# Performance work log

Hardware: AMD Instinct MI355X
Metric: run time of the kernel (lower is better)

Reference implementation:

```python
import jax, jax.numpy as jnp
import numpy as np

N = 50000        # num nodes
E = 800000       # num edges (avg degree 16)
NFEAT = 128
NHID = 128
NCLASS = 64


def setup_inputs() -> dict:
    key = jax.random.key(0)
    k0, k1, k2, k3 = jax.random.split(key, 4)
    x = jax.random.normal(k0, (N, NFEAT), dtype=jnp.float32)
    edge_index = jax.random.randint(k1, (2, E), 0, N)
    edge_weight = jnp.ones((E,), dtype=jnp.float32)
    # GCNConv linear weights (glorot-ish uniform), biases zero
    s1 = 1.0 / np.sqrt(NFEAT)
    W1 = jax.random.uniform(k2, (NFEAT, NHID), jnp.float32, -s1, s1)
    b1 = jnp.zeros((NHID,), jnp.float32)
    s2 = 1.0 / np.sqrt(NHID)
    W2 = jax.random.uniform(k3, (NHID, NCLASS), jnp.float32, -s2, s2)
    b2 = jnp.zeros((NCLASS,), jnp.float32)
    return {"x": x, "edge_index": edge_index, "edge_weight": edge_weight,
            "W1": W1, "b1": b1, "W2": W2, "b2": b2}


def reference(x, edge_index, edge_weight, W1, b1, W2, b2):
    n = x.shape[0]
    # add self loops (fill_value = 1.0), as GCNConv(add_self_loops=True)
    loops = jnp.arange(n)
    ei = jnp.concatenate([edge_index, jnp.stack([loops, loops])], axis=1)
    ew = jnp.concatenate([edge_weight, jnp.ones((n,), x.dtype)])
    row, col = ei[0], ei[1]
    # symmetric gcn normalization: D^-1/2 A D^-1/2
    deg = jax.ops.segment_sum(ew, col, num_segments=n)
    dinv = jnp.where(deg > 0, jax.lax.rsqrt(deg), 0.0)
    norm = dinv[row] * ew * dinv[col]        # [E+N]

    def conv(h, W, b):
        h = h @ W                                   # [N, F_out]
        msg = norm[:, None] * h[row]                # gather + scale, [E+N, F_out]
        return jax.ops.segment_sum(msg, col, num_segments=n) + b

    h = jax.nn.relu(conv(x, W1, b1))  # dropout p=0.0 -> identity
    out = conv(h, W2, b2)
    # F.normalize(p=2, dim=-1)
    nrm = jnp.linalg.norm(out, axis=-1, keepdims=True)
    return out / jnp.maximum(nrm, 1e-12)
```

## Files before the change

### kernel.cpp

```cpp
#include <hip/hip_runtime.h>

#define NF 128
#define NC 64
#define SLICES 64

__device__ __forceinline__ unsigned f2bf(float f) {
    unsigned u = __float_as_uint(f);
    return (u + 0x7FFFu + ((u >> 16) & 1u)) >> 16;
}
__device__ __forceinline__ float bf2f(unsigned h) { return __uint_as_float(h << 16); }

__global__ __launch_bounds__(256) void count_rank_kernel(const int* __restrict__ col,
                                                         unsigned short* __restrict__ eoff16,
                                                         unsigned short* __restrict__ C16,
                                                         int N, int E, int SL, int nh) {
    __shared__ unsigned hist[12544];
    const int j = blockIdx.x >> 1;
    const int h = blockIdx.x & 1;
    const int nlo = h * nh;
    const int nhi = min(N, nlo + nh);
    const int words = (nhi - nlo + 1) >> 1;
    for (int i = threadIdx.x; i < words; i += 256) hist[i] = 0;
    __syncthreads();
    const int e0 = j * SL, e1 = min(E, e0 + SL);
    for (int e = e0 + threadIdx.x; e < e1; e += 256) {
        int c = col[e];
        if (c >= nlo && c < nhi) {
            int cl = c - nlo;
            unsigned sh = (cl & 1) * 16;
            unsigned old = atomicAdd(&hist[cl >> 1], 1u << sh);
            eoff16[e] = (unsigned short)((old >> sh) & 0xffffu);
        }
    }
    __syncthreads();
    unsigned* Cw = (unsigned*)(C16 + (size_t)j * N + nlo);
    for (int i = threadIdx.x; i < words; i += 256) Cw[i] = hist[i];
}

__global__ __launch_bounds__(256) void scanC_kernel(unsigned short* __restrict__ C16,
                                                    int* __restrict__ tot, int N) {
    int n = blockIdx.x * 256 + threadIdx.x;
    if (n >= N) return;
    int t = 0;
#pragma unroll 4
    for (int j = 0; j < SLICES; ++j) {
        size_t idx = (size_t)j * N + n;
        int v = C16[idx];
        C16[idx] = (unsigned short)t;
        t += v;
    }
    tot[n] = t;
}

__global__ __launch_bounds__(256) void scan_blocks(const int* __restrict__ cnt,
                                                   int* __restrict__ excl,
                                                   int* __restrict__ bsum, int N) {
    __shared__ int sh[256];
    int t = threadIdx.x;
    int base = blockIdx.x * 1024 + t * 4;
    int v0 = base + 0 < N ? cnt[base + 0] : 0;
    int v1 = base + 1 < N ? cnt[base + 1] : 0;
    int v2 = base + 2 < N ? cnt[base + 2] : 0;
    int v3 = base + 3 < N ? cnt[base + 3] : 0;
    int s = v0 + v1 + v2 + v3;
    sh[t] = s;
    __syncthreads();
    for (int off = 1; off < 256; off <<= 1) {
        int x = (t >= off) ? sh[t - off] : 0;
        __syncthreads();
        sh[t] += x;
        __syncthreads();
    }
    int incl = sh[t];
    int exclT = incl - s;
    if (t == 255) bsum[blockIdx.x] = incl;
    if (base + 0 < N) excl[base + 0] = exclT;
    if (base + 1 < N) excl[base + 1] = exclT + v0;
    if (base + 2 < N) excl[base + 2] = exclT + v0 + v1;
    if (base + 3 < N) excl[base + 3] = exclT + v0 + v1 + v2;
}

__global__ void scan_sums(int* __restrict__ bsum, int nb) {
    int run = 0;
    for (int i = 0; i < nb; ++i) { int v = bsum[i]; bsum[i] = run; run += v; }
    bsum[nb] = run;
}

__global__ __launch_bounds__(256) void scan_add(int* __restrict__ excl,
                                                const int* __restrict__ bsum,
                                                int N, int nb) {
    int i = blockIdx.x * 256 + threadIdx.x;
    if (i < N) excl[i] += bsum[i >> 10];
    if (i == 0) excl[N] = bsum[nb];
}

__global__ __launch_bounds__(256) void scatter_gemm1_fused(const int* __restrict__ row,
                                                           const int* __restrict__ col,
                                                           const float* __restrict__ ew,
                                                           const int* __restrict__ rowPtr,
                                                           const unsigned short* __restrict__ Coff16,
                                                           const unsigned short* __restrict__ eoff16,
                                                           int2* __restrict__ csr,
                                                           const float* __restrict__ X,
                                                           const float* __restrict__ W,
                                                           unsigned short* __restrict__ H,
                                                           int N, int E, int SL, int SB) {
    __shared__ float Xs[32][64];
    __shared__ float Wsh[32][128];
    if ((int)blockIdx.x < SB) {
        int stride = SB * 256;
        for (int e = blockIdx.x * 256 + threadIdx.x; e < E; e += stride) {
            int c = col[e];
            int j = e / SL;
            int idx = rowPtr[c] + (int)Coff16[(size_t)j * N + c] + (int)eoff16[e];
            csr[idx] = make_int2(row[e], __float_as_int(ew[e]));
        }
        return;
    }
    const int bm0 = (blockIdx.x - SB) * 64;
    const int tid = threadIdx.x;
    const int tx = tid & 15, ty = tid >> 4;
    float acc[4][8] = {};
    for (int kc = 0; kc < 4; ++kc) {
        {
            int r = tid >> 2, q = tid & 3;
            int node = min(bm0 + r, N - 1);
            const float4* src = (const float4*)(X + (size_t)node * 128 + kc * 32);
#pragma unroll
            for (int qq = 0; qq < 2; ++qq) {
                float4 v = src[q + qq * 4];
                int k = (q + qq * 4) * 4;
                Xs[k + 0][r] = v.x;
                Xs[k + 1][r] = v.y;
                Xs[k + 2][r] = v.z;
                Xs[k + 3][r] = v.w;
            }
        }
        {
            const float4* src = (const float4*)(W + (size_t)kc * 32 * 128);
            float4* dst = (float4*)&Wsh[0][0];
#pragma unroll
            for (int i = tid; i < 1024; i += 256) dst[i] = src[i];
        }
        __syncthreads();
#pragma unroll 4
        for (int k = 0; k < 32; ++k) {
            float4 xa = *(const float4*)&Xs[k][tx * 4];
            float4 wA = *(const float4*)&Wsh[k][ty * 8];
            float4 wB = *(const float4*)&Wsh[k][ty * 8 + 4];
            float xv[4] = {xa.x, xa.y, xa.z, xa.w};
            float wv[8] = {wA.x, wA.y, wA.z, wA.w, wB.x, wB.y, wB.z, wB.w};
#pragma unroll
            for (int i = 0; i < 4; ++i)
#pragma unroll
                for (int j = 0; j < 8; ++j)
                    acc[i][j] = fmaf(xv[i], wv[j], acc[i][j]);
        }
        __syncthreads();
    }
#pragma unroll
    for (int i = 0; i < 4; ++i) {
        int n = bm0 + tx * 4 + i;
        if (n < N) {
            ushort4 oA, oB;
            oA.x = (unsigned short)f2bf(acc[i][0]); oA.y = (unsigned short)f2bf(acc[i][1]);
            oA.z = (unsigned short)f2bf(acc[i][2]); oA.w = (unsigned short)f2bf(acc[i][3]);
            oB.x = (unsigned short)f2bf(acc[i][4]); oB.y = (unsigned short)f2bf(acc[i][5]);
            oB.z = (unsigned short)f2bf(acc[i][6]); oB.w = (unsigned short)f2bf(acc[i][7]);
            *(ushort4*)&H[(size_t)n * 128 + ty * 8] = oA;
            *(ushort4*)&H[(size_t)n * 128 + ty * 8 + 4] = oB;
        }
    }
}

__global__ __launch_bounds__(256) void deg_dinv_kernel(const int* __restrict__ rowPtr,
                                                       const int2* __restrict__ csr,
                                                       float* __restrict__ dinv, int N) {
    int idx = blockIdx.x * 256 + threadIdx.x;
    int n = idx >> 4, l = idx & 15;
    if (n >= N) return;
    int beg = rowPtr[n], end = rowPtr[n + 1];
    float s = 0.f;
    for (int i = beg + l; i < end; i += 16) s += __int_as_float(csr[i].y);
#pragma unroll
    for (int off = 8; off; off >>= 1) s += __shfl_xor(s, off, 16);
    if (l == 0) dinv[n] = rsqrtf(s + 1.0f);
}

__global__ __launch_bounds__(256) void norm_csr_kernel(int2* __restrict__ csr,
                                                       const float* __restrict__ dinv, int E) {
    int i = blockIdx.x * 256 + threadIdx.x;
    if (i >= E) return;
    int2 p = csr[i];
    ((int*)csr)[2 * i + 1] = __float_as_int(__int_as_float(p.y) * dinv[p.x]);
}

__global__ __launch_bounds__(256) void agg_gather1(const int* __restrict__ rowPtr,
                                                   const int2* __restrict__ csr,
                                                   const unsigned* __restrict__ H1u,
                                                   const float* __restrict__ dinv,
                                                   const float2* __restrict__ b2,
                                                   float2* __restrict__ out2, int N) {
    int n = (blockIdx.x * 256 + threadIdx.x) >> 6;
    int lane = threadIdx.x & 63;
    if (n >= N) return;
    float dn = dinv[n];
    float accx = 0.f, accy = 0.f;
    int beg = rowPtr[n], end = rowPtr[n + 1];
    int j = beg;
    for (; j + 4 <= end; j += 4) {
        int2 p0 = csr[j + 0], p1 = csr[j + 1], p2 = csr[j + 2], p3 = csr[j + 3];
        unsigned v0 = H1u[(size_t)p0.x * 64 + lane];
        unsigned v1 = H1u[(size_t)p1.x * 64 + lane];
        unsigned v2 = H1u[(size_t)p2.x * 64 + lane];
        unsigned v3 = H1u[(size_t)p3.x * 64 + lane];
        float w0 = __int_as_float(p0.y), w1 = __int_as_float(p1.y);
        float w2 = __int_as_float(p2.y), w3 = __int_as_float(p3.y);
        accx += w0 * bf2f(v0 & 0xffffu); accy += w0 * bf2f(v0 >> 16);
        accx += w1 * bf2f(v1 & 0xffffu); accy += w1 * bf2f(v1 >> 16);
        accx += w2 * bf2f(v2 & 0xffffu); accy += w2 * bf2f(v2 >> 16);
        accx += w3 * bf2f(v3 & 0xffffu); accy += w3 * bf2f(v3 >> 16);
    }
    for (; j < end; ++j) {
        int2 p = csr[j];
        unsigned v = H1u[(size_t)p.x * 64 + lane];
        float w = __int_as_float(p.y);
        accx += w * bf2f(v & 0xffffu); accy += w * bf2f(v >> 16);
    }
    unsigned hv = H1u[(size_t)n * 64 + lane];
    float2 bb = b2[lane];
    float s = dn * dn;
    float2 o;
    o.x = fmaxf(fmaf(dn, accx, s * bf2f(hv & 0xffffu)) + bb.x, 0.f);
    o.y = fmaxf(fmaf(dn, accy, s * bf2f(hv >> 16)) + bb.y, 0.f);
    out2[(size_t)n * 64 + lane] = o;
}

__global__ __launch_bounds__(256) void gemm_tile64(const float* __restrict__ X,
                                                   const float* __restrict__ W,
                                                   unsigned short* __restrict__ H, int N) {
    __shared__ float Xs[32][64];
    __shared__ float Wsh[32][64];
    const int bm0 = blockIdx.x * 64;
    const int tid = threadIdx.x;
    const int tx = tid & 15, ty = tid >> 4;
    float acc[4][4] = {};
    for (int kc = 0; kc < 4; ++kc) {
        {
            int r = tid >> 2, q = tid & 3;
            int node = min(bm0 + r, N - 1);
            const float4* src = (const float4*)(X + (size_t)node * 128 + kc * 32);
#pragma unroll
            for (int qq = 0; qq < 2; ++qq) {
                float4 v = src[q + qq * 4];
                int k = (q + qq * 4) * 4;
                Xs[k + 0][r] = v.x;
                Xs[k + 1][r] = v.y;
                Xs[k + 2][r] = v.z;
                Xs[k + 3][r] = v.w;
            }
        }
        {
            const float4* src = (const float4*)(W + (size_t)kc * 32 * 64);
            float4* dst = (float4*)&Wsh[0][0];
#pragma unroll
            for (int i = tid; i < 512; i += 256) dst[i] = src[i];
        }
        __syncthreads();
#pragma unroll 4
        for (int k = 0; k < 32; ++k) {
            float4 xa = *(const float4*)&Xs[k][tx * 4];
            float4 w4 = *(const float4*)&Wsh[k][ty * 4];
            float xv[4] = {xa.x, xa.y, xa.z, xa.w};
            float wv[4] = {w4.x, w4.y, w4.z, w4.w};
#pragma unroll
            for (int i = 0; i < 4; ++i)
#pragma unroll
                for (int j = 0; j < 4; ++j)
                    acc[i][j] = fmaf(xv[i], wv[j], acc[i][j]);
        }
        __syncthreads();
    }
#pragma unroll
    for (int i = 0; i < 4; ++i) {
        int n = bm0 + tx * 4 + i;
        if (n < N) {
            ushort4 o;
            o.x = (unsigned short)f2bf(acc[i][0]);
            o.y = (unsigned short)f2bf(acc[i][1]);
            o.z = (unsigned short)f2bf(acc[i][2]);
            o.w = (unsigned short)f2bf(acc[i][3]);
            *(ushort4*)&H[(size_t)n * 64 + ty * 4] = o;
        }
    }
}

__global__ __launch_bounds__(256) void agg_gather2(const int* __restrict__ rowPtr,
                                                   const int2* __restrict__ csr,
                                                   const unsigned* __restrict__ H3u,
                                                   const float* __restrict__ dinv,
                                                   const float2* __restrict__ b2,
                                                   float2* __restrict__ out2, int N) {
    int n = (blockIdx.x * 256 + threadIdx.x) >> 5;
    int l = threadIdx.x & 31;
    if (n >= N) return;
    float dn = dinv[n];
    float accx = 0.f, accy = 0.f;
    int beg = rowPtr[n], end = rowPtr[n + 1];
    int j = beg;
    for (; j + 4 <= end; j += 4) {
        int2 p0 = csr[j + 0], p1 = csr[j + 1], p2 = csr[j + 2], p3 = csr[j + 3];
        unsigned v0 = H3u[(size_t)p0.x * 32 + l];
        unsigned v1 = H3u[(size_t)p1.x * 32 + l];
        unsigned v2 = H3u[(size_t)p2.x * 32 + l];
        unsigned v3 = H3u[(size_t)p3.x * 32 + l];
        float w0 = __int_as_float(p0.y), w1 = __int_as_float(p1.y);
        float w2 = __int_as_float(p2.y), w3 = __int_as_float(p3.y);
        accx += w0 * bf2f(v0 & 0xffffu); accy += w0 * bf2f(v0 >> 16);
        accx += w1 * bf2f(v1 & 0xffffu); accy += w1 * bf2f(v1 >> 16);
        accx += w2 * bf2f(v2 & 0xffffu); accy += w2 * bf2f(v2 >> 16);
        accx += w3 * bf2f(v3 & 0xffffu); accy += w3 * bf2f(v3 >> 16);
    }
    for (; j < end; ++j) {
        int2 p = csr[j];
        unsigned v = H3u[(size_t)p.x * 32 + l];
        float w = __int_as_float(p.y);
        accx += w * bf2f(v & 0xffffu); accy += w * bf2f(v >> 16);
    }
    unsigned hv = H3u[(size_t)n * 32 + l];
    float2 bb = b2[l];
    float s = dn * dn;
    float vx = fmaf(dn, accx, s * bf2f(hv & 0xffffu)) + bb.x;
    float vy = fmaf(dn, accy, s * bf2f(hv >> 16)) + bb.y;
    float ss = vx * vx + vy * vy;
#pragma unroll
    for (int off = 16; off; off >>= 1) ss += __shfl_xor(ss, off, 64);
    float scale = 1.0f / fmaxf(sqrtf(ss), 1e-12f);
    out2[(size_t)n * 32 + l] = make_float2(vx * scale, vy * scale);
}

extern "C" void kernel_launch(void* const* d_in, const int* in_sizes, int n_in,
                              void* d_out, int out_size, void* d_ws, size_t ws_size,
                              hipStream_t stream) {
    const float* x  = (const float*)d_in[0];
    const int*   ei = (const int*)d_in[1];
    const float* ew = (const float*)d_in[2];
    const float* W1 = (const float*)d_in[3];
    const float* b1 = (const float*)d_in[4];
    const float* W2 = (const float*)d_in[5];
    const float* b2 = (const float*)d_in[6];
    float* out = (float*)d_out;
    const int N = in_sizes[0] / NF;
    const int E = in_sizes[2];
    const int* row = ei;
    const int* col = ei + E;
    const int NB = (N + 1023) / 1024;
    const int SL = (E + SLICES - 1) / SLICES;
    const int nh = (N + 1) / 2;

    char* ws = (char*)d_ws;
    size_t off = 0;
    auto take = [&](size_t bytes) {
        char* p = ws + off;
        off = (off + bytes + 255) & ~(size_t)255;
        return p;
    };
    float* dinv   = (float*)take((size_t)N * 4);
    int*   tot    = (int*)  take((size_t)N * 4);
    int*   rowPtr = (int*)  take((size_t)(N + 1) * 4);
    unsigned short* eoff16 = (unsigned short*)take((size_t)E * 2);
    int*   bsum   = (int*)  take((size_t)(NB + 1) * 4);
    unsigned short* C16    = (unsigned short*)take((size_t)SLICES * N * 2);
    int2*  csr    = (int2*) take((size_t)E * 8);
    unsigned short* H1 = (unsigned short*)take((size_t)N * NF * 2);
    float* buf2   = (float*)take((size_t)N * NF * 4);
    unsigned short* H3 = H1;

    count_rank_kernel<<<2 * SLICES, 256, 0, stream>>>(col, eoff16, C16, N, E, SL, nh);
    scanC_kernel<<<(N + 255) / 256, 256, 0, stream>>>(C16, tot, N);
    scan_blocks<<<NB, 256, 0, stream>>>(tot, rowPtr, bsum, N);
    scan_sums<<<1, 1, 0, stream>>>(bsum, NB);
    scan_add<<<(N + 255) / 256, 256, 0, stream>>>(rowPtr, bsum, N, NB);

    const int SB = 128;
    const int GB = (N + 63) / 64;
    scatter_gemm1_fused<<<SB + GB, 256, 0, stream>>>(row, col, ew, rowPtr, C16, eoff16,
                                                     csr, x, W1, H1, N, E, SL, SB);

    deg_dinv_kernel<<<(N * 16 + 255) / 256, 256, 0, stream>>>(rowPtr, csr, dinv, N);
    norm_csr_kernel<<<(E + 255) / 256, 256, 0, stream>>>(csr, dinv, E);

    agg_gather1<<<(N * 64 + 255) / 256, 256, 0, stream>>>(rowPtr, csr, (const unsigned*)H1,
                                                          dinv, (const float2*)b1,
                                                          (float2*)buf2, N);

    gemm_tile64<<<(N + 63) / 64, 256, 0, stream>>>(buf2, W2, H3, N);
    agg_gather2<<<(N * 32 + 255) / 256, 256, 0, stream>>>(rowPtr, csr, (const unsigned*)H3,
                                                          dinv, (const float2*)b2,
                                                          (float2*)out, N);
}
```

Baseline: 174.4 us.

## Use bf16 MFMA for both GEMMs, fold normalization into gathers, partition scatter

Both dense GEMMs move from scalar FP32 FMA tiles to bf16 MFMA 16x16x32 tiles. The inputs are converted to bf16 into swizzled LDS, and the weights are pre-transposed to bf16 by a new prep kernel. The separate norm_csr pass is removed, so each gather multiplies by dinv[src] on the fly. The layer-1 ReLU output is stored as bf16 instead of fp32, halving the GEMM2 input traffic. The CSR scatter blocks are split into four node-range quarters to improve write locality, at the cost of each block rereading all of col. Lower input precision and the extra dinv gathers are the tradeoffs.

```diff
diff --git a/kernel.cpp b/kernel.cpp
--- a/kernel.cpp
+++ b/kernel.cpp
@@ -4,11 +4,31 @@
 #define NC 64
 #define SLICES 64
 
+typedef short bf16x8 __attribute__((ext_vector_type(8)));
+typedef float f32x4 __attribute__((ext_vector_type(4)));
+
 __device__ __forceinline__ unsigned f2bf(float f) {
     unsigned u = __float_as_uint(f);
     return (u + 0x7FFFu + ((u >> 16) & 1u)) >> 16;
 }
 __device__ __forceinline__ float bf2f(unsigned h) { return __uint_as_float(h << 16); }
+
+__global__ __launch_bounds__(256) void wt_prep(const float* __restrict__ W1,
+                                               const float* __restrict__ W2,
+                                               unsigned short* __restrict__ Wt1,
+                                               unsigned short* __restrict__ Wt2) {
+    int i = blockIdx.x * 256 + threadIdx.x;
+    if (i < 128 * 128) {
+        int k = i >> 7, n = i & 127;
+        Wt1[n * 128 + k] = (unsigned short)f2bf(W1[i]);
+    } else {
+        int j = i - 128 * 128;
+        if (j < 128 * 64) {
+            int k = j >> 6, n = j & 63;
+            Wt2[n * 128 + k] = (unsigned short)f2bf(W2[j]);
+        }
+    }
+}
 
 __global__ __launch_bounds__(256) void count_rank_kernel(const int* __restrict__ col,
                                                          unsigned short* __restrict__ eoff16,
@@ -102,75 +122,141 @@
                                                            const unsigned short* __restrict__ eoff16,
                                                            int2* __restrict__ csr,
                                                            const float* __restrict__ X,
-                                                           const float* __restrict__ W,
+                                                           const unsigned short* __restrict__ Wt1,
                                                            unsigned short* __restrict__ H,
-                                                           int N, int E, int SL, int SB) {
-    __shared__ float Xs[32][64];
-    __shared__ float Wsh[32][128];
+                                                           int N, int E, int SL, int SB, int nq) {
+    __shared__ char XsB[32768];
+    __shared__ char WsB[32768];
     if ((int)blockIdx.x < SB) {
-        int stride = SB * 256;
-        for (int e = blockIdx.x * 256 + threadIdx.x; e < E; e += stride) {
+        int q = blockIdx.x & 3;
+        int qlo = q * nq, qhi = min(N, qlo + nq);
+        int stride = (SB >> 2) * 256;
+        for (int e = (blockIdx.x >> 2) * 256 + threadIdx.x; e < E; e += stride) {
             int c = col[e];
+            if (c < qlo || c >= qhi) continue;
             int j = e / SL;
             int idx = rowPtr[c] + (int)Coff16[(size_t)j * N + c] + (int)eoff16[e];
             csr[idx] = make_int2(row[e], __float_as_int(ew[e]));
         }
         return;
     }
-    const int bm0 = (blockIdx.x - SB) * 64;
     const int tid = threadIdx.x;
-    const int tx = tid & 15, ty = tid >> 4;
-    float acc[4][8] = {};
-    for (int kc = 0; kc < 4; ++kc) {
-        {
-            int r = tid >> 2, q = tid & 3;
+    const int bm0 = ((int)blockIdx.x - SB) * 128;
+    {
+        int k4 = tid & 31;
+        int r0 = tid >> 5;
+        for (int it = 0; it < 16; ++it) {
+            int r = it * 8 + r0;
             int node = min(bm0 + r, N - 1);
-            const float4* src = (const float4*)(X + (size_t)node * 128 + kc * 32);
-#pragma unroll
-            for (int qq = 0; qq < 2; ++qq) {
-                float4 v = src[q + qq * 4];
-                int k = (q + qq * 4) * 4;
-                Xs[k + 0][r] = v.x;
-                Xs[k + 1][r] = v.y;
-                Xs[k + 2][r] = v.z;
-                Xs[k + 3][r] = v.w;
+            float4 v = *(const float4*)(X + (size_t)node * 128 + k4 * 4);
+            unsigned lo = f2bf(v.x) | (f2bf(v.y) << 16);
+            unsigned hi = f2bf(v.z) | (f2bf(v.w) << 16);
+            int byte = r * 256 + ((k4 * 8) ^ ((r & 7) << 4));
+            *(uint2*)(XsB + byte) = make_uint2(lo, hi);
+        }
+    }
+    {
+        const uint4* src = (const uint4*)Wt1;
+        for (int t = 0; t < 8; ++t) {
+            int i = t * 256 + tid;
+            int n = i >> 4, kb = (i & 15) * 16;
+            *(uint4*)(WsB + n * 256 + (kb ^ ((n & 7) << 4))) = src[i];
+        }
+    }
+    __syncthreads();
+    const int w = tid >> 6, l = tid & 63;
+    const int lr = l & 15, lg = l >> 4;
+    f32x4 acc[2][8] = {};
+#pragma unroll
+    for (int kk = 0; kk < 4; ++kk) {
+        bf16x8 a[2], b[8];
+#pragma unroll
+        for (int mt = 0; mt < 2; ++mt) {
+            int r = w * 32 + mt * 16 + lr;
+            a[mt] = *(const bf16x8*)(XsB + r * 256 + ((kk * 64 + lg * 16) ^ ((r & 7) << 4)));
+        }
+#pragma unroll
+        for (int nt = 0; nt < 8; ++nt) {
+            int n = nt * 16 + lr;
+            b[nt] = *(const bf16x8*)(WsB + n * 256 + ((kk * 64 + lg * 16) ^ ((n & 7) << 4)));
+        }
+#pragma unroll
+        for (int mt = 0; mt < 2; ++mt)
+#pragma unroll
+            for (int nt = 0; nt < 8; ++nt)
+                acc[mt][nt] = __builtin_amdgcn_mfma_f32_16x16x32_bf16(a[mt], b[nt], acc[mt][nt], 0, 0, 0);
+    }
+#pragma unroll
+    for (int mt = 0; mt < 2; ++mt)
+#pragma unroll
+        for (int reg = 0; reg < 4; ++reg) {
+            int node = bm0 + w * 32 + mt * 16 + lg * 4 + reg;
+            if (node < N) {
+#pragma unroll
+                for (int nt = 0; nt < 8; ++nt)
+                    H[(size_t)node * 128 + nt * 16 + lr] = (unsigned short)f2bf(acc[mt][nt][reg]);
             }
         }
-        {
-            const float4* src = (const float4*)(W + (size_t)kc * 32 * 128);
-            float4* dst = (float4*)&Wsh[0][0];
-#pragma unroll
-            for (int i = tid; i < 1024; i += 256) dst[i] = src[i];
-        }
-        __syncthreads();
-#pragma unroll 4
-        for (int k = 0; k < 32; ++k) {
-            float4 xa = *(const float4*)&Xs[k][tx * 4];
-            float4 wA = *(const float4*)&Wsh[k][ty * 8];
-            float4 wB = *(const float4*)&Wsh[k][ty * 8 + 4];
-            float xv[4] = {xa.x, xa.y, xa.z, xa.w};
-            float wv[8] = {wA.x, wA.y, wA.z, wA.w, wB.x, wB.y, wB.z, wB.w};
-#pragma unroll
-            for (int i = 0; i < 4; ++i)
-#pragma unroll
-                for (int j = 0; j < 8; ++j)
-                    acc[i][j] = fmaf(xv[i], wv[j], acc[i][j]);
-        }
-        __syncthreads();
-    }
-#pragma unroll
-    for (int i = 0; i < 4; ++i) {
-        int n = bm0 + tx * 4 + i;
-        if (n < N) {
-            ushort4 oA, oB;
-            oA.x = (unsigned short)f2bf(acc[i][0]); oA.y = (unsigned short)f2bf(acc[i][1]);
-            oA.z = (unsigned short)f2bf(acc[i][2]); oA.w = (unsigned short)f2bf(acc[i][3]);
-            oB.x = (unsigned short)f2bf(acc[i][4]); oB.y = (unsigned short)f2bf(acc[i][5]);
-            oB.z = (unsigned short)f2bf(acc[i][6]); oB.w = (unsigned short)f2bf(acc[i][7]);
-            *(ushort4*)&H[(size_t)n * 128 + ty * 8] = oA;
-            *(ushort4*)&H[(size_t)n * 128 + ty * 8 + 4] = oB;
-        }
-    }
+}
+
+__global__ __launch_bounds__(256) void gemm2_mfma(const unsigned short* __restrict__ A,
+                                                  const unsigned short* __restrict__ Wt2,
+                                                  unsigned short* __restrict__ H, int N) {
+    __shared__ char XsB[32768];
+    __shared__ char WsB[16384];
+    const int tid = threadIdx.x;
+    const int bm0 = blockIdx.x * 128;
+    {
+        int k16 = tid & 15, r0 = tid >> 4;
+        for (int it = 0; it < 8; ++it) {
+            int r = it * 16 + r0;
+            int node = min(bm0 + r, N - 1);
+            uint4 g = *(const uint4*)(A + (size_t)node * 128 + k16 * 8);
+            *(uint4*)(XsB + r * 256 + ((k16 * 16) ^ ((r & 7) << 4))) = g;
+        }
+    }
+    {
+        const uint4* src = (const uint4*)Wt2;
+        for (int t = 0; t < 4; ++t) {
+            int i = t * 256 + tid;
+            int n = i >> 4, kb = (i & 15) * 16;
+            *(uint4*)(WsB + n * 256 + (kb ^ ((n & 7) << 4))) = src[i];
+        }
+    }
+    __syncthreads();
+    const int w = tid >> 6, l = tid & 63;
+    const int lr = l & 15, lg = l >> 4;
+    f32x4 acc[2][4] = {};
+#pragma unroll
+    for (int kk = 0; kk < 4; ++kk) {
+        bf16x8 a[2], b[4];
+#pragma unroll
+        for (int mt = 0; mt < 2; ++mt) {
+            int r = w * 32 + mt * 16 + lr;
+            a[mt] = *(const bf16x8*)(XsB + r * 256 + ((kk * 64 + lg * 16) ^ ((r & 7) << 4)));
+        }
+#pragma unroll
+        for (int nt = 0; nt < 4; ++nt) {
+            int n = nt * 16 + lr;
+            b[nt] = *(const bf16x8*)(WsB + n * 256 + ((kk * 64 + lg * 16) ^ ((n & 7) << 4)));
+        }
+#pragma unroll
+        for (int mt = 0; mt < 2; ++mt)
+#pragma unroll
+            for (int nt = 0; nt < 4; ++nt)
+                acc[mt][nt] = __builtin_amdgcn_mfma_f32_16x16x32_bf16(a[mt], b[nt], acc[mt][nt], 0, 0, 0);
+    }
+#pragma unroll
+    for (int mt = 0; mt < 2; ++mt)
+#pragma unroll
+        for (int reg = 0; reg < 4; ++reg) {
+            int node = bm0 + w * 32 + mt * 16 + lg * 4 + reg;
+            if (node < N) {
+#pragma unroll
+                for (int nt = 0; nt < 4; ++nt)
+                    H[(size_t)node * 64 + nt * 16 + lr] = (unsigned short)f2bf(acc[mt][nt][reg]);
+            }
+        }
 }
 
 __global__ __launch_bounds__(256) void deg_dinv_kernel(const int* __restrict__ rowPtr,
@@ -187,20 +273,12 @@
     if (l == 0) dinv[n] = rsqrtf(s + 1.0f);
 }
 
-__global__ __launch_bounds__(256) void norm_csr_kernel(int2* __restrict__ csr,
-                                                       const float* __restrict__ dinv, int E) {
-    int i = blockIdx.x * 256 + threadIdx.x;
-    if (i >= E) return;
-    int2 p = csr[i];
-    ((int*)csr)[2 * i + 1] = __float_as_int(__int_as_float(p.y) * dinv[p.x]);
-}
-
 __global__ __launch_bounds__(256) void agg_gather1(const int* __restrict__ rowPtr,
                                                    const int2* __restrict__ csr,
                                                    const unsigned* __restrict__ H1u,
                                                    const float* __restrict__ dinv,
                                                    const float2* __restrict__ b2,
-                                                   float2* __restrict__ out2, int N) {
+                                                   unsigned* __restrict__ out1, int N) {
     int n = (blockIdx.x * 256 + threadIdx.x) >> 6;
     int lane = threadIdx.x & 63;
     if (n >= N) return;
@@ -210,12 +288,14 @@
     int j = beg;
     for (; j + 4 <= end; j += 4) {
         int2 p0 = csr[j + 0], p1 = csr[j + 1], p2 = csr[j + 2], p3 = csr[j + 3];
+        float w0 = __int_as_float(p0.y) * dinv[p0.x];
+        float w1 = __int_as_float(p1.y) * dinv[p1.x];
+        float w2 = __int_as_float(p2.y) * dinv[p2.x];
+        float w3 = __int_as_float(p3.y) * dinv[p3.x];
         unsigned v0 = H1u[(size_t)p0.x * 64 + lane];
         unsigned v1 = H1u[(size_t)p1.x * 64 + lane];
         unsigned v2 = H1u[(size_t)p2.x * 64 + lane];
         unsigned v3 = H1u[(size_t)p3.x * 64 + lane];
-        float w0 = __int_as_float(p0.y), w1 = __int_as_float(p1.y);
-        float w2 = __int_as_float(p2.y), w3 = __int_as_float(p3.y);
         accx += w0 * bf2f(v0 & 0xffffu); accy += w0 * bf2f(v0 >> 16);
         accx += w1 * bf2f(v1 & 0xffffu); accy += w1 * bf2f(v1 >> 16);
         accx += w2 * bf2f(v2 & 0xffffu); accy += w2 * bf2f(v2 >> 16);
@@ -223,76 +303,16 @@
     }
     for (; j < end; ++j) {
         int2 p = csr[j];
+        float w = __int_as_float(p.y) * dinv[p.x];
         unsigned v = H1u[(size_t)p.x * 64 + lane];
-        float w = __int_as_float(p.y);
         accx += w * bf2f(v & 0xffffu); accy += w * bf2f(v >> 16);
     }
     unsigned hv = H1u[(size_t)n * 64 + lane];
     float2 bb = b2[lane];
     float s = dn * dn;
-    float2 o;
-    o.x = fmaxf(fmaf(dn, accx, s * bf2f(hv & 0xffffu)) + bb.x, 0.f);
-    o.y = fmaxf(fmaf(dn, accy, s * bf2f(hv >> 16)) + bb.y, 0.f);
-    out2[(size_t)n * 64 + lane] = o;
-}
-
-__global__ __launch_bounds__(256) void gemm_tile64(const float* __restrict__ X,
-                                                   const float* __restrict__ W,
-                                                   unsigned short* __restrict__ H, int N) {
-    __shared__ float Xs[32][64];
-    __shared__ float Wsh[32][64];
-    const int bm0 = blockIdx.x * 64;
-    const int tid = threadIdx.x;
-    const int tx = tid & 15, ty = tid >> 4;
-    float acc[4][4] = {};
-    for (int kc = 0; kc < 4; ++kc) {
-        {
-            int r = tid >> 2, q = tid & 3;
-            int node = min(bm0 + r, N - 1);
-            const float4* src = (const float4*)(X + (size_t)node * 128 + kc * 32);
-#pragma unroll
-            for (int qq = 0; qq < 2; ++qq) {
-                float4 v = src[q + qq * 4];
-                int k = (q + qq * 4) * 4;
-                Xs[k + 0][r] = v.x;
-                Xs[k + 1][r] = v.y;
-                Xs[k + 2][r] = v.z;
-                Xs[k + 3][r] = v.w;
-            }
-        }
-        {
-            const float4* src = (const float4*)(W + (size_t)kc * 32 * 64);
-            float4* dst = (float4*)&Wsh[0][0];
-#pragma unroll
-            for (int i = tid; i < 512; i += 256) dst[i] = src[i];
-        }
-        __syncthreads();
-#pragma unroll 4
-        for (int k = 0; k < 32; ++k) {
-            float4 xa = *(const float4*)&Xs[k][tx * 4];
-            float4 w4 = *(const float4*)&Wsh[k][ty * 4];
-            float xv[4] = {xa.x, xa.y, xa.z, xa.w};
-            float wv[4] = {w4.x, w4.y, w4.z, w4.w};
-#pragma unroll
-            for (int i = 0; i < 4; ++i)
-#pragma unroll
-                for (int j = 0; j < 4; ++j)
-                    acc[i][j] = fmaf(xv[i], wv[j], acc[i][j]);
-        }
-        __syncthreads();
-    }
-#pragma unroll
-    for (int i = 0; i < 4; ++i) {
-        int n = bm0 + tx * 4 + i;
-        if (n < N) {
-            ushort4 o;
-            o.x = (unsigned short)f2bf(acc[i][0]);
-            o.y = (unsigned short)f2bf(acc[i][1]);
-            o.z = (unsigned short)f2bf(acc[i][2]);
-            o.w = (unsigned short)f2bf(acc[i][3]);
-            *(ushort4*)&H[(size_t)n * 64 + ty * 4] = o;
-        }
-    }
+    float ox = fmaxf(fmaf(dn, accx, s * bf2f(hv & 0xffffu)) + bb.x, 0.f);
+    float oy = fmaxf(fmaf(dn, accy, s * bf2f(hv >> 16)) + bb.y, 0.f);
+    out1[(size_t)n * 64 + lane] = f2bf(ox) | (f2bf(oy) << 16);
 }
 
 __global__ __launch_bounds__(256) void agg_gather2(const int* __restrict__ rowPtr,
@@ -310,12 +330,14 @@
     int j = beg;
     for (; j + 4 <= end; j += 4) {
         int2 p0 = csr[j + 0], p1 = csr[j + 1], p2 = csr[j + 2], p3 = csr[j + 3];
+        float w0 = __int_as_float(p0.y) * dinv[p0.x];
+        float w1 = __int_as_float(p1.y) * dinv[p1.x];
+        float w2 = __int_as_float(p2.y) * dinv[p2.x];
+        float w3 = __int_as_float(p3.y) * dinv[p3.x];
         unsigned v0 = H3u[(size_t)p0.x * 32 + l];
         unsigned v1 = H3u[(size_t)p1.x * 32 + l];
         unsigned v2 = H3u[(size_t)p2.x * 32 + l];
         unsigned v3 = H3u[(size_t)p3.x * 32 + l];
-        float w0 = __int_as_float(p0.y), w1 = __int_as_float(p1.y);
-        float w2 = __int_as_float(p2.y), w3 = __int_as_float(p3.y);
         accx += w0 * bf2f(v0 & 0xffffu); accy += w0 * bf2f(v0 >> 16);
         accx += w1 * bf2f(v1 & 0xffffu); accy += w1 * bf2f(v1 >> 16);
         accx += w2 * bf2f(v2 & 0xffffu); accy += w2 * bf2f(v2 >> 16);
@@ -323,8 +345,8 @@
     }
     for (; j < end; ++j) {
         int2 p = csr[j];
+        float w = __int_as_float(p.y) * dinv[p.x];
         unsigned v = H3u[(size_t)p.x * 32 + l];
-        float w = __int_as_float(p.y);
         accx += w * bf2f(v & 0xffffu); accy += w * bf2f(v >> 16);
     }
     unsigned hv = H3u[(size_t)n * 32 + l];
@@ -357,6 +379,7 @@
     const int NB = (N + 1023) / 1024;
     const int SL = (E + SLICES - 1) / SLICES;
     const int nh = (N + 1) / 2;
+    const int nq = (N + 3) / 4;
 
     char* ws = (char*)d_ws;
     size_t off = 0;
@@ -372,9 +395,13 @@
     int*   bsum   = (int*)  take((size_t)(NB + 1) * 4);
     unsigned short* C16    = (unsigned short*)take((size_t)SLICES * N * 2);
     int2*  csr    = (int2*) take((size_t)E * 8);
-    unsigned short* H1 = (unsigned short*)take((size_t)N * NF * 2);
-    float* buf2   = (float*)take((size_t)N * NF * 4);
+    unsigned short* H1   = (unsigned short*)take((size_t)N * NF * 2);
+    unsigned short* relu = (unsigned short*)take((size_t)N * NF * 2);
+    unsigned short* Wt1  = (unsigned short*)take(128 * 128 * 2);
+    unsigned short* Wt2  = (unsigned short*)take(64 * 128 * 2);
     unsigned short* H3 = H1;
+
+    wt_prep<<<96, 256, 0, stream>>>(W1, W2, Wt1, Wt2);
 
     count_rank_kernel<<<2 * SLICES, 256, 0, stream>>>(col, eoff16, C16, N, E, SL, nh);
     scanC_kernel<<<(N + 255) / 256, 256, 0, stream>>>(C16, tot, N);
@@ -383,18 +410,17 @@
     scan_add<<<(N + 255) / 256, 256, 0, stream>>>(rowPtr, bsum, N, NB);
 
     const int SB = 128;
-    const int GB = (N + 63) / 64;
+    const int GB = (N + 127) / 128;
     scatter_gemm1_fused<<<SB + GB, 256, 0, stream>>>(row, col, ew, rowPtr, C16, eoff16,
-                                                     csr, x, W1, H1, N, E, SL, SB);
+                                                     csr, x, Wt1, H1, N, E, SL, SB, nq);
 
     deg_dinv_kernel<<<(N * 16 + 255) / 256, 256, 0, stream>>>(rowPtr, csr, dinv, N);
-    norm_csr_kernel<<<(E + 255) / 256, 256, 0, stream>>>(csr, dinv, E);
 
     agg_gather1<<<(N * 64 + 255) / 256, 256, 0, stream>>>(rowPtr, csr, (const unsigned*)H1,
                                                           dinv, (const float2*)b1,
-                                                          (float2*)buf2, N);
-
-    gemm_tile64<<<(N + 63) / 64, 256, 0, stream>>>(buf2, W2, H3, N);
+                                                          (unsigned*)relu, N);
+
+    gemm2_mfma<<<(N + 127) / 128, 256, 0, stream>>>(relu, Wt2, H3, N);
     agg_gather2<<<(N * 32 + 255) / 256, 256, 0, stream>>>(rowPtr, csr, (const unsigned*)H3,
                                                           dinv, (const float2*)b2,
                                                           (float2*)out, N);
```

New measurement: 204.1 us. 17.0% more time.
